# Kernel optimization log

Measured on AMD Instinct MI355X. Metric: run time of the kernel, lower is better.

Reference implementation:

```python
import jax, jax.numpy as jnp
import numpy as np
from jax import lax

B, V, H, W = 8, 3, 512, 640


def setup_inputs() -> dict:
    key = jax.random.key(0)
    k1, k2, k3 = jax.random.split(key, 3)
    # predicted depths in a realistic positive range
    pred_pts = jax.random.uniform(k1, (B, V, H, W), jnp.float32, 1.0, 10.0)
    # pinhole intrinsics embedded in 4x4 (invertible)
    f = 500.0
    K1 = jnp.array([[f, 0.0, (W - 1) / 2.0, 0.0],
                    [0.0, f, (H - 1) / 2.0, 0.0],
                    [0.0, 0.0, 1.0, 0.0],
                    [0.0, 0.0, 0.0, 1.0]], jnp.float32)
    K = jnp.broadcast_to(K1, (B, 4, 4))
    # near-identity rotations (QR of I + small noise) + small translations
    A = jnp.eye(3, dtype=jnp.float32) + 0.05 * jax.random.normal(k2, (B, V, 3, 3), jnp.float32)
    Q, R = jnp.linalg.qr(A)
    Q = Q * jnp.sign(jnp.diagonal(R, axis1=-2, axis2=-1))[..., None, :]
    t = 0.1 * jax.random.normal(k3, (B, V, 3), jnp.float32)
    RT = (jnp.zeros((B, V, 4, 4), jnp.float32)
          .at[..., :3, :3].set(Q)
          .at[..., :3, 3].set(t)
          .at[..., 3, 3].set(1.0))
    return {"pred_pts": pred_pts, "K": K, "input_RTs": RT}


def _bilinear_sample(img_flat, gx, gy, h, w):
    """grid_sample(mode=bilinear, align_corners=False, padding=zeros).
    img_flat: (B, H*W); gx, gy: (B, N) in [-1, 1] grid coords."""
    ix = ((gx + 1.0) * w - 1.0) * 0.5
    iy = ((gy + 1.0) * h - 1.0) * 0.5
    x0f = jnp.floor(ix)
    y0f = jnp.floor(iy)
    wx1 = ix - x0f
    wy1 = iy - y0f
    x0 = x0f.astype(jnp.int32)
    y0 = y0f.astype(jnp.int32)

    def corner(xi, yi):
        valid = (xi >= 0) & (xi < w) & (yi >= 0) & (yi < h)
        idx = jnp.clip(yi, 0, h - 1) * w + jnp.clip(xi, 0, w - 1)
        val = jnp.take_along_axis(img_flat, idx, axis=1)
        return jnp.where(valid, val, 0.0)

    return ((1.0 - wy1) * (1.0 - wx1) * corner(x0, y0)
            + (1.0 - wy1) * wx1 * corner(x0 + 1, y0)
            + wy1 * (1.0 - wx1) * corner(x0, y0 + 1)
            + wy1 * wx1 * corner(x0 + 1, y0 + 1))


def reference(pred_pts, K, input_RTs):
    b, v, h, w = pred_pts.shape
    dt = pred_pts.dtype
    yy, xx = jnp.meshgrid(jnp.arange(h, dtype=dt), jnp.arange(w, dtype=dt), indexing='ij')
    x = xx.reshape(-1)  # (HW,)
    y = yy.reshape(-1)
    Kinv = jnp.linalg.inv(K)            # (B,4,4)
    RTinv = jnp.linalg.inv(input_RTs)   # (B,V,4,4)

    total = jnp.zeros((), dt)
    for i in range(v):
        for j in range(v):
            d = pred_pts[:, i].reshape(b, -1)          # (B, HW)
            ones = jnp.ones_like(d)
            # homogeneous coords (x*d, y*d, d, 1): (B, 4, HW)
            xyz = jnp.stack([x[None] * d, y[None] * d, d, ones], axis=1)
            # composed projection: K @ RT_j @ inv(RT_i) @ inv(K)  (same math as chained bmms)
            P = jnp.einsum('bij,bjk,bkl,blm->bim', K, input_RTs[:, j], RTinv[:, i], Kinv)
            proj = jnp.einsum('bij,bjn->bin', P, xyz)  # (B, 4, HW)
            proj = proj / proj[:, 3:4]
            projected_depth = proj[:, 2]               # (B, HW)
            gx = proj[:, 0] / ((w - 1) / 2.0) - 1.0
            gy = proj[:, 1] / ((h - 1) / 2.0) - 1.0
            mask = ((gx >= -1.0) & (gx <= 1.0) & (gy >= -1.0) & (gy <= 1.0)).astype(dt)
            warped = _bilinear_sample(pred_pts[:, j].reshape(b, -1), gx, gy, h, w)
            num = jnp.sum(jnp.abs(warped - projected_depth) * mask)
            den = jnp.maximum(jnp.sum(mask), 1.0)
            total = total + num / den
    return total
```

## Files before the change

### kernel.cpp

```cpp
#include <hip/hip_runtime.h>

#define Bn 8
#define Vn 3
#define Hn 512
#define Wn 640
#define Nn (Hn * Wn)
#define PX 16
#define TPB 256
#define XBLKS (Nn / (TPB * PX))
#define GRIDN (XBLKS * Vn * Bn)

struct __attribute__((aligned(4))) fpair { float a, b; };

__device__ __forceinline__ float rfl(float x) {
    return __int_as_float(__builtin_amdgcn_readfirstlane(__float_as_int(x)));
}

__device__ __forceinline__ void computeQ(const float* __restrict__ K,
                                         const float* __restrict__ RT,
                                         int b, int i, float Q[Vn][12]) {
    const float* Kb = K + (size_t)b * 16;
    const float f  = Kb[0], cx = Kb[2], cy = Kb[6];
    const float rf = 1.0f / f;
    const float* Ti = RT + (size_t)(b * Vn + i) * 16;
    const float A00=Ti[0], A01=Ti[1], A02=Ti[2],  A03=Ti[3];
    const float A10=Ti[4], A11=Ti[5], A12=Ti[6],  A13=Ti[7];
    const float A20=Ti[8], A21=Ti[9], A22=Ti[10], A23=Ti[11];
    const float I00=A00, I01=A10, I02=A20, I03=-(A00*A03 + A10*A13 + A20*A23);
    const float I10=A01, I11=A11, I12=A21, I13=-(A01*A03 + A11*A13 + A21*A23);
    const float I20=A02, I21=A12, I22=A22, I23=-(A02*A03 + A12*A13 + A22*A23);
    #pragma unroll
    for (int j = 0; j < Vn; ++j) {
        const float* Tj = RT + (size_t)(b * Vn + j) * 16;
        const float B00=Tj[0], B01=Tj[1], B02=Tj[2],  B03=Tj[3];
        const float B10=Tj[4], B11=Tj[5], B12=Tj[6],  B13=Tj[7];
        const float B20=Tj[8], B21=Tj[9], B22=Tj[10], B23=Tj[11];
        const float M00=B00*I00+B01*I10+B02*I20, M01=B00*I01+B01*I11+B02*I21,
                    M02=B00*I02+B01*I12+B02*I22, M03=B00*I03+B01*I13+B02*I23+B03;
        const float M10=B10*I00+B11*I10+B12*I20, M11=B10*I01+B11*I11+B12*I21,
                    M12=B10*I02+B11*I12+B12*I22, M13=B10*I03+B11*I13+B12*I23+B13;
        const float M20=B20*I00+B21*I10+B22*I20, M21=B20*I01+B21*I11+B22*I21,
                    M22=B20*I02+B21*I12+B22*I22, M23=B20*I03+B21*I13+B22*I23+B23;
        const float G00=f*M00+cx*M20, G01=f*M01+cx*M21, G02=f*M02+cx*M22, G03=f*M03+cx*M23;
        const float G10=f*M10+cy*M20, G11=f*M11+cy*M21, G12=f*M12+cy*M22, G13=f*M13+cy*M23;
        const float G20=M20,          G21=M21,          G22=M22,          G23=M23;
        Q[j][0]  = rfl(G00*rf);  Q[j][1]  = rfl(G01*rf);
        Q[j][2]  = rfl(G02 - (cx*rf)*G00 - (cy*rf)*G01);  Q[j][3]  = rfl(G03);
        Q[j][4]  = rfl(G10*rf);  Q[j][5]  = rfl(G11*rf);
        Q[j][6]  = rfl(G12 - (cx*rf)*G10 - (cy*rf)*G11);  Q[j][7]  = rfl(G13);
        Q[j][8]  = rfl(G20*rf);  Q[j][9]  = rfl(G21*rf);
        Q[j][10] = rfl(G22 - (cx*rf)*G20 - (cy*rf)*G21);  Q[j][11] = rfl(G23);
    }
}

__global__ __launch_bounds__(TPB, 8) void loss_main_kernel(const float* __restrict__ pred,
                                                           const float* __restrict__ K,
                                                           const float* __restrict__ RT,
                                                           float* __restrict__ accum) {
    const int id   = blockIdx.x;
    const int b    = id & 7;
    const int r    = id >> 3;
    const int i    = r % Vn;
    const int xblk = r / Vn;

    float Q[Vn][12];
    computeQ(K, RT, b, i, Q);

    const int p    = threadIdx.x * XBLKS + xblk;
    const int base = p * PX;
    const int yrow = base / Wn;
    const int xcol = base - yrow * Wn;
    const float fy = (float)yrow;

    const float* dptr = pred + (size_t)(b * Vn + i) * Nn + base;
    float dv[PX];
    {
        const float4 a0 = *reinterpret_cast<const float4*>(dptr);
        const float4 a1 = *reinterpret_cast<const float4*>(dptr + 4);
        const float4 a2 = *reinterpret_cast<const float4*>(dptr + 8);
        const float4 a3 = *reinterpret_cast<const float4*>(dptr + 12);
        dv[0]=a0.x; dv[1]=a0.y; dv[2]=a0.z; dv[3]=a0.w;
        dv[4]=a1.x; dv[5]=a1.y; dv[6]=a1.z; dv[7]=a1.w;
        dv[8]=a2.x; dv[9]=a2.y; dv[10]=a2.z; dv[11]=a2.w;
        dv[12]=a3.x; dv[13]=a3.y; dv[14]=a3.z; dv[15]=a3.w;
    }

    const float cW = (float)Wn / (float)(Wn - 1);
    const float cH = (float)Hn / (float)(Hn - 1);

    float num[Vn] = {0.0f, 0.0f, 0.0f};
    float den[Vn] = {0.0f, 0.0f, 0.0f};

    #pragma unroll
    for (int j = 0; j < Vn; ++j) {
        const float* __restrict__ img = pred + (size_t)(b * Vn + j) * Nn;
        const float rx = fmaf(Q[j][1], fy, Q[j][2]);
        const float ry = fmaf(Q[j][5], fy, Q[j][6]);
        const float rz = fmaf(Q[j][9], fy, Q[j][10]);

        #pragma unroll
        for (int k = 0; k < PX; ++k) {
            const float d  = dv[k];
            const float fx = (float)(xcol + k);

            const float X = fmaf(d, fmaf(Q[j][0], fx, rx), Q[j][3]);
            const float Y = fmaf(d, fmaf(Q[j][4], fx, ry), Q[j][7]);
            const float Z = fmaf(d, fmaf(Q[j][8], fx, rz), Q[j][11]);

            const bool inb = (X >= 0.0f) & (X <= (float)(Wn - 1)) &
                             (Y >= 0.0f) & (Y <= (float)(Hn - 1));
            if (inb) {
                const float ix = fmaf(X, cW, -0.5f);
                const float iy = fmaf(Y, cH, -0.5f);
                const float x0f = floorf(ix);
                const float y0f = floorf(iy);
                const float wx1 = ix - x0f;
                const float wy1 = iy - y0f;
                const float wx0 = 1.0f - wx1;
                const float wy0 = 1.0f - wy1;
                const int x0 = (int)x0f;
                const int y0 = (int)y0f;
                const int x1 = x0 + 1;
                const int y1 = y0 + 1;
                const int cy0 = max(y0, 0);
                const int cy1 = min(y1, Hn - 1);

                const int cx   = min(max(x0, 0), Wn - 2);
                const bool xlo = (x0 >= 0);
                const bool xhi = (x0 <= Wn - 2);
                const fpair q0 = *reinterpret_cast<const fpair*>(img + (cy0 * Wn + cx));
                const fpair q1 = *reinterpret_cast<const fpair*>(img + (cy1 * Wn + cx));
                const float c00 = xhi ? q0.a : q0.b;
                const float c10 = xlo ? q0.b : q0.a;
                const float c01 = xhi ? q1.a : q1.b;
                const float c11 = xlo ? q1.b : q1.a;

                const float wx0v = xlo ? wx0 : 0.0f;
                const float wx1v = (x1 < Wn) ? wx1 : 0.0f;
                const float wy0v = (y0 >= 0) ? wy0 : 0.0f;
                const float wy1v = (y1 < Hn) ? wy1 : 0.0f;

                const float warped = wy0v * fmaf(wx0v, c00, wx1v * c10)
                                   + wy1v * fmaf(wx0v, c01, wx1v * c11);
                num[j] += fabsf(warped - Z);
                den[j] += 1.0f;
            }
        }
    }

    #pragma unroll
    for (int off = 32; off > 0; off >>= 1) {
        #pragma unroll
        for (int j = 0; j < Vn; ++j) {
            num[j] += __shfl_down(num[j], off, 64);
            den[j] += __shfl_down(den[j], off, 64);
        }
    }
    __shared__ float s_red[4][2 * Vn];
    const int lane = threadIdx.x & 63;
    const int wid  = threadIdx.x >> 6;
    if (lane == 0) {
        #pragma unroll
        for (int j = 0; j < Vn; ++j) {
            s_red[wid][2 * j + 0] = num[j];
            s_red[wid][2 * j + 1] = den[j];
        }
    }
    __syncthreads();
    if (threadIdx.x < 2 * Vn) {
        const int slot = threadIdx.x;
        const float v = s_red[0][slot] + s_red[1][slot] + s_red[2][slot] + s_red[3][slot];
        const int j = slot >> 1;
        const int comp = slot & 1;
        atomicAdd(&accum[(i * Vn + j) * 2 + comp], v);
    }
}

__global__ void finalize_kernel(const float* __restrict__ accum, float* __restrict__ out) {
    if (threadIdx.x == 0 && blockIdx.x == 0) {
        float t = 0.0f;
        for (int pr = 0; pr < Vn * Vn; ++pr) {
            t += accum[pr * 2 + 0] / fmaxf(accum[pr * 2 + 1], 1.0f);
        }
        out[0] = t;
    }
}

extern "C" void kernel_launch(void* const* d_in, const int* in_sizes, int n_in,
                              void* d_out, int out_size, void* d_ws, size_t ws_size,
                              hipStream_t stream) {
    const float* pred = (const float*)d_in[0];
    const float* K    = (const float*)d_in[1];
    const float* RT   = (const float*)d_in[2];
    float* out = (float*)d_out;

    float* accum = (float*)d_ws;

    hipMemsetAsync(d_ws, 0, 128, stream);
    loss_main_kernel<<<GRIDN, TPB, 0, stream>>>(pred, K, RT, accum);
    finalize_kernel<<<1, 64, 0, stream>>>(accum, out);
}
```

Measured before the change: 121.9 us.

## Add wave-uniform interior fast path and replace atomics with per-block partials

The bilinear gather now takes a simplified path with no clamping whenever no lane in the wavefront has a border sample, checked with a ballot. Only wavefronts that touch the border run the full clamped logic. Global atomics and the memset are replaced by per-block partial sums written to the workspace, which a 256-thread finalize kernel reduces. This removes the memset launch and atomic contention, at the cost of a slightly larger final reduction.

```diff
diff --git a/kernel.cpp b/kernel.cpp
--- a/kernel.cpp
+++ b/kernel.cpp
@@ -56,7 +56,7 @@
 __global__ __launch_bounds__(TPB, 8) void loss_main_kernel(const float* __restrict__ pred,
                                                            const float* __restrict__ K,
                                                            const float* __restrict__ RT,
-                                                           float* __restrict__ accum) {
+                                                           float* __restrict__ part) {
     const int id   = blockIdx.x;
     const int b    = id & 7;
     const int r    = id >> 3;
@@ -120,28 +120,35 @@
                 const float wy0 = 1.0f - wy1;
                 const int x0 = (int)x0f;
                 const int y0 = (int)y0f;
-                const int x1 = x0 + 1;
-                const int y1 = y0 + 1;
-                const int cy0 = max(y0, 0);
-                const int cy1 = min(y1, Hn - 1);
-
-                const int cx   = min(max(x0, 0), Wn - 2);
-                const bool xlo = (x0 >= 0);
-                const bool xhi = (x0 <= Wn - 2);
-                const fpair q0 = *reinterpret_cast<const fpair*>(img + (cy0 * Wn + cx));
-                const fpair q1 = *reinterpret_cast<const fpair*>(img + (cy1 * Wn + cx));
-                const float c00 = xhi ? q0.a : q0.b;
-                const float c10 = xlo ? q0.b : q0.a;
-                const float c01 = xhi ? q1.a : q1.b;
-                const float c11 = xlo ? q1.b : q1.a;
-
-                const float wx0v = xlo ? wx0 : 0.0f;
-                const float wx1v = (x1 < Wn) ? wx1 : 0.0f;
-                const float wy0v = (y0 >= 0) ? wy0 : 0.0f;
-                const float wy1v = (y1 < Hn) ? wy1 : 0.0f;
-
-                const float warped = wy0v * fmaf(wx0v, c00, wx1v * c10)
-                                   + wy1v * fmaf(wx0v, c01, wx1v * c11);
+                const bool border = (x0 < 0) | (x0 > Wn - 2) | (y0 < 0) | (y0 > Hn - 2);
+                float warped;
+                if (__ballot(border) == 0ull) {
+                    const int ad = y0 * Wn + x0;
+                    const fpair q0 = *reinterpret_cast<const fpair*>(img + ad);
+                    const fpair q1 = *reinterpret_cast<const fpair*>(img + ad + Wn);
+                    warped = wy0 * fmaf(wx0, q0.a, wx1 * q0.b)
+                           + wy1 * fmaf(wx0, q1.a, wx1 * q1.b);
+                } else {
+                    const int x1 = x0 + 1;
+                    const int y1 = y0 + 1;
+                    const int cy0 = max(y0, 0);
+                    const int cy1 = min(y1, Hn - 1);
+                    const int cx  = min(max(x0, 0), Wn - 2);
+                    const bool xlo = (x0 >= 0);
+                    const bool xhi = (x0 <= Wn - 2);
+                    const fpair q0 = *reinterpret_cast<const fpair*>(img + (cy0 * Wn + cx));
+                    const fpair q1 = *reinterpret_cast<const fpair*>(img + (cy1 * Wn + cx));
+                    const float c00 = xhi ? q0.a : q0.b;
+                    const float c10 = xlo ? q0.b : q0.a;
+                    const float c01 = xhi ? q1.a : q1.b;
+                    const float c11 = xlo ? q1.b : q1.a;
+                    const float wx0v = xlo ? wx0 : 0.0f;
+                    const float wx1v = (x1 < Wn) ? wx1 : 0.0f;
+                    const float wy0v = (y0 >= 0) ? wy0 : 0.0f;
+                    const float wy1v = (y1 < Hn) ? wy1 : 0.0f;
+                    warped = wy0v * fmaf(wx0v, c00, wx1v * c10)
+                           + wy1v * fmaf(wx0v, c01, wx1v * c11);
+                }
                 num[j] += fabsf(warped - Z);
                 den[j] += 1.0f;
             }
@@ -170,17 +177,46 @@
     if (threadIdx.x < 2 * Vn) {
         const int slot = threadIdx.x;
         const float v = s_red[0][slot] + s_red[1][slot] + s_red[2][slot] + s_red[3][slot];
-        const int j = slot >> 1;
-        const int comp = slot & 1;
-        atomicAdd(&accum[(i * Vn + j) * 2 + comp], v);
-    }
-}
-
-__global__ void finalize_kernel(const float* __restrict__ accum, float* __restrict__ out) {
-    if (threadIdx.x == 0 && blockIdx.x == 0) {
+        part[(size_t)id * 8 + slot] = v;
+    }
+}
+
+__global__ __launch_bounds__(TPB) void finalize_kernel(const float* __restrict__ part,
+                                                       float* __restrict__ out) {
+    float acc[2 * Vn * Vn];
+    #pragma unroll
+    for (int s = 0; s < 2 * Vn * Vn; ++s) acc[s] = 0.0f;
+
+    for (int m = threadIdx.x; m < GRIDN; m += TPB) {
+        const int i = (m >> 3) % Vn;
+        const float* pp = part + (size_t)m * 8;
+        #pragma unroll
+        for (int j = 0; j < Vn; ++j) {
+            acc[(i * Vn + j) * 2 + 0] += pp[2 * j + 0];
+            acc[(i * Vn + j) * 2 + 1] += pp[2 * j + 1];
+        }
+    }
+    #pragma unroll
+    for (int off = 32; off > 0; off >>= 1) {
+        #pragma unroll
+        for (int s = 0; s < 2 * Vn * Vn; ++s)
+            acc[s] += __shfl_down(acc[s], off, 64);
+    }
+    __shared__ float s_fin[4][2 * Vn * Vn];
+    const int lane = threadIdx.x & 63;
+    const int wid  = threadIdx.x >> 6;
+    if (lane == 0) {
+        #pragma unroll
+        for (int s = 0; s < 2 * Vn * Vn; ++s) s_fin[wid][s] = acc[s];
+    }
+    __syncthreads();
+    if (threadIdx.x == 0) {
         float t = 0.0f;
+        #pragma unroll
         for (int pr = 0; pr < Vn * Vn; ++pr) {
-            t += accum[pr * 2 + 0] / fmaxf(accum[pr * 2 + 1], 1.0f);
+            const float nn = s_fin[0][pr*2+0] + s_fin[1][pr*2+0] + s_fin[2][pr*2+0] + s_fin[3][pr*2+0];
+            const float dd = s_fin[0][pr*2+1] + s_fin[1][pr*2+1] + s_fin[2][pr*2+1] + s_fin[3][pr*2+1];
+            t += nn / fmaxf(dd, 1.0f);
         }
         out[0] = t;
     }
@@ -194,9 +230,8 @@
     const float* RT   = (const float*)d_in[2];
     float* out = (float*)d_out;
 
-    float* accum = (float*)d_ws;
-
-    hipMemsetAsync(d_ws, 0, 128, stream);
-    loss_main_kernel<<<GRIDN, TPB, 0, stream>>>(pred, K, RT, accum);
-    finalize_kernel<<<1, 64, 0, stream>>>(accum, out);
-}
+    float* part = (float*)d_ws;
+
+    loss_main_kernel<<<GRIDN, TPB, 0, stream>>>(pred, K, RT, part);
+    finalize_kernel<<<1, TPB, 0, stream>>>(part, out);
+}
```

Result: faster. 111.4 us (median of 2 runs) (-8.7%).
